# Optimization experiments

Hardware: AMD Instinct MI355X
Metric: run time of the kernel (lower is better)

## Reference

```python
import jax, jax.numpy as jnp
import numpy as np

D, H, O, E, K = 1024, 4096, 1024, 12, 4
N = 8192


def setup_inputs() -> dict:
    key = jax.random.key(0)
    ks = jax.random.split(key, 7)
    s = 0.02
    return {
        "x": jax.random.normal(ks[0], (N, D), dtype=jnp.float32),
        "gate_w": jax.random.normal(ks[1], (D, E), dtype=jnp.float32) * s,
        "gate_b": jnp.zeros((E,), dtype=jnp.float32),
        "w1": jax.random.normal(ks[2], (E, D, H), dtype=jnp.float32) * s,
        "b1": jnp.zeros((E, H), dtype=jnp.float32),
        "w2": jax.random.normal(ks[3], (E, H, O), dtype=jnp.float32) * s,
        "b2": jnp.zeros((E, O), dtype=jnp.float32),
    }


def reference(x, gate_w, gate_b, w1, b1, w2, b2):
    # Gating: full softmax over all experts, then mask to top-k and renormalize
    scores = x @ gate_w + gate_b                      # [N, E]
    _, topk_idx = jax.lax.top_k(scores, K)            # [N, K]
    mask = jnp.sum(jax.nn.one_hot(topk_idx, E, dtype=scores.dtype), axis=-2)  # [N, E]
    weights = jax.nn.softmax(scores, axis=-1) * mask
    weights = weights / (jnp.sum(weights, axis=-1, keepdims=True) + 1e-8)

    # Dense all-expert MLP (faithful to original: every expert on every token)
    h = jax.nn.relu(jnp.einsum("nd,edh->neh", x, w1) + b1)  # [N, E, H]
    outs = jnp.einsum("neh,eho->neo", h, w2) + b2           # [N, E, O]

    return jnp.einsum("ne,neo->no", weights, outs)          # [N, O]
```

## Files before the change

### kernel.cpp

```cpp
#include <hip/hip_runtime.h>
#include <stdint.h>

#define D_DIM 1024
#define H_DIM 4096
#define O_DIM 1024
#define E_NUM 12
#define TOPK 4
#define N_TOK 8192

#define PAIR_CAP 36096

typedef __bf16 bf16x8 __attribute__((ext_vector_type(8)));
typedef float f32x4 __attribute__((ext_vector_type(4)));
typedef unsigned short u16x8 __attribute__((ext_vector_type(8)));

typedef __attribute__((address_space(3))) unsigned int lds_uint;
typedef __attribute__((address_space(1))) const unsigned int glob_uint;

static __device__ __forceinline__ unsigned short f2b(float f) {
  union { float f; unsigned u; } v; v.f = f;
  unsigned r = v.u + 0x7FFFu + ((v.u >> 16) & 1u);
  return (unsigned short)(r >> 16);
}

static __device__ __forceinline__ void gload16(const void* g, void* l) {
  __builtin_amdgcn_global_load_lds((glob_uint*)g, (lds_uint*)l, 16, 0, 0);
}

__global__ __launch_bounds__(256) void cvt_x_kernel(const float* __restrict__ x,
                                                    unsigned short* __restrict__ xb) {
  int i = blockIdx.x * 256 + threadIdx.x;
  const float4* p = reinterpret_cast<const float4*>(x);
  float4 a = p[2 * i], b = p[2 * i + 1];
  uint4 st;
  st.x = (unsigned)f2b(a.x) | ((unsigned)f2b(a.y) << 16);
  st.y = (unsigned)f2b(a.z) | ((unsigned)f2b(a.w) << 16);
  st.z = (unsigned)f2b(b.x) | ((unsigned)f2b(b.y) << 16);
  st.w = (unsigned)f2b(b.z) | ((unsigned)f2b(b.w) << 16);
  reinterpret_cast<uint4*>(xb)[i] = st;
}

__global__ __launch_bounds__(256) void transpose_cvt_kernel(const float* __restrict__ in,
                                                            unsigned short* __restrict__ out,
                                                            int R, int C) {
  __shared__ float tile[64][33];
  int e = blockIdx.z;
  size_t base = (size_t)e * R * C;
  int c0 = blockIdx.x * 32, r0 = blockIdx.y * 64;
  int tx = threadIdx.x & 31, ty = threadIdx.x >> 5;
#pragma unroll
  for (int i = 0; i < 64; i += 8)
    tile[ty + i][tx] = in[base + (size_t)(r0 + ty + i) * C + (c0 + tx)];
  __syncthreads();
#pragma unroll
  for (int k = 0; k < 4; k++) {
    int c = ty + k * 8;
    unsigned lo = f2b(tile[2 * tx][c]);
    unsigned hi = f2b(tile[2 * tx + 1][c]);
    *reinterpret_cast<unsigned*>(&out[base + (size_t)(c0 + c) * R + r0 + 2 * tx]) =
        lo | (hi << 16);
  }
}

__global__ __launch_bounds__(256) void gwt_kernel(const float* __restrict__ gw,
                                                  float* __restrict__ gwT) {
  int e = blockIdx.x;
#pragma unroll
  for (int i = 0; i < 4; i++) {
    int d = i * 256 + threadIdx.x;
    gwT[e * D_DIM + d] = gw[(size_t)d * E_NUM + e];
  }
}

__global__ __launch_bounds__(256) void gating_kernel(const float* __restrict__ x,
                                                     const float* __restrict__ gwT,
                                                     const float* __restrict__ gb,
                                                     int* __restrict__ tk_e,
                                                     float* __restrict__ tk_w) {
  int wv = (blockIdx.x * 256 + threadIdx.x) >> 6;
  int lane = threadIdx.x & 63;
  int n0 = wv * 4;
  if (n0 >= N_TOK) return;

  const float4* x4 = reinterpret_cast<const float4*>(x);
  const float4* g4 = reinterpret_cast<const float4*>(gwT);

  float acc[4][E_NUM];
#pragma unroll
  for (int t = 0; t < 4; t++)
#pragma unroll
    for (int e = 0; e < E_NUM; e++) acc[t][e] = 0.f;

#pragma unroll
  for (int i = 0; i < 4; i++) {
    float4 xv[4];
#pragma unroll
    for (int t = 0; t < 4; t++) xv[t] = x4[(size_t)(n0 + t) * 256 + i * 64 + lane];
#pragma unroll
    for (int e = 0; e < E_NUM; e++) {
      float4 g = g4[e * 256 + i * 64 + lane];
#pragma unroll
      for (int t = 0; t < 4; t++)
        acc[t][e] += xv[t].x * g.x + xv[t].y * g.y + xv[t].z * g.z + xv[t].w * g.w;
    }
  }

#pragma unroll
  for (int t = 0; t < 4; t++)
#pragma unroll
    for (int e = 0; e < E_NUM; e++) {
      float v = acc[t][e];
#pragma unroll
      for (int s = 32; s > 0; s >>= 1) v += __shfl_xor(v, s, 64);
      acc[t][e] = v;
    }

#pragma unroll
  for (int t = 0; t < 4; t++) {
    if (lane == t) {
      int n = n0 + t;
      float sc[E_NUM], sm[E_NUM];
      float mx = -1e30f;
#pragma unroll
      for (int e = 0; e < E_NUM; e++) { sc[e] = acc[t][e] + gb[e]; mx = fmaxf(mx, sc[e]); }
      float Z = 0.f;
#pragma unroll
      for (int e = 0; e < E_NUM; e++) { sm[e] = expf(sc[e] - mx); Z += sm[e]; }
      bool used[E_NUM];
#pragma unroll
      for (int e = 0; e < E_NUM; e++) used[e] = false;
      int eid[TOPK]; float p[TOPK]; float wsum = 0.f;
      for (int k = 0; k < TOPK; k++) {
        float best = -1e30f; int bi = 0;
        for (int e = 0; e < E_NUM; e++)
          if (!used[e] && sc[e] > best) { best = sc[e]; bi = e; }
        used[bi] = true; eid[k] = bi; p[k] = sm[bi] / Z; wsum += p[k];
      }
      float inv = 1.f / (wsum + 1e-8f);
      for (int k = 0; k < TOPK; k++) {
        tk_e[n * TOPK + k] = eid[k];
        tk_w[n * TOPK + k] = p[k] * inv;
      }
    }
  }
}

__global__ __launch_bounds__(256) void hist_rank_kernel(const int* __restrict__ tk_e,
                                                        int* __restrict__ lr,
                                                        int* __restrict__ bc) {
  int blk = blockIdx.x, t = threadIdx.x;
  int n = blk * 256 + t;
  int4 te = reinterpret_cast<const int4*>(tk_e)[n];
  int lane = t & 63, w = t >> 6;
  __shared__ int wt[4][E_NUM];
  int r0 = 0, r1 = 0, r2 = 0, r3 = 0;
#pragma unroll
  for (int e = 0; e < E_NUM; e++) {
    int flag = (te.x == e) || (te.y == e) || (te.z == e) || (te.w == e);
    unsigned long long m = __ballot(flag);
    int rw = __popcll(m & ((1ull << lane) - 1ull));
    if (lane == 0) wt[w][e] = __popcll(m);
    if (te.x == e) r0 = rw;
    if (te.y == e) r1 = rw;
    if (te.z == e) r2 = rw;
    if (te.w == e) r3 = rw;
  }
  __syncthreads();
#pragma unroll
  for (int e = 0; e < E_NUM; e++) {
    int base = 0;
#pragma unroll
    for (int w2 = 0; w2 < 4; w2++)
      if (w2 < w) base += wt[w2][e];
    if (te.x == e) r0 += base;
    if (te.y == e) r1 += base;
    if (te.z == e) r2 += base;
    if (te.w == e) r3 += base;
  }
  int4 out; out.x = r0; out.y = r1; out.z = r2; out.w = r3;
  reinterpret_cast<int4*>(lr)[n] = out;
  if (t == 0) {
#pragma unroll
    for (int e = 0; e < E_NUM; e++)
      bc[blk * E_NUM + e] = wt[0][e] + wt[1][e] + wt[2][e] + wt[3][e];
  }
}

__global__ __launch_bounds__(64) void scan2_kernel(const int* __restrict__ bc,
                                                   int* __restrict__ poff,
                                                   int* __restrict__ bb) {
  int t = threadIdx.x;
  __shared__ int cnte[E_NUM];
  __shared__ int spoff[E_NUM + 1];
  if (t < E_NUM) {
    int s = 0;
#pragma unroll
    for (int b = 0; b < 32; b++) s += bc[b * E_NUM + t];
    cnte[t] = s;
  }
  __syncthreads();
  if (t == 0) {
    int off = 0; spoff[0] = 0;
    for (int e = 0; e < E_NUM; e++) {
      off += ((cnte[e] + 255) >> 8) << 8;
      spoff[e + 1] = off;
    }
  }
  __syncthreads();
  if (t < E_NUM + 1) poff[t] = spoff[t];
  if (t < E_NUM) {
    int run = spoff[t];
    for (int b = 0; b < 32; b++) {
      bb[b * E_NUM + t] = run;
      run += bc[b * E_NUM + t];
    }
  }
}

__global__ __launch_bounds__(256) void fill_pairs_kernel(int* __restrict__ pt) {
  int i = blockIdx.x * 256 + threadIdx.x;
  if (i < PAIR_CAP) pt[i] = 0;
}

__global__ __launch_bounds__(256) void scatter2_kernel(const int* __restrict__ tk_e,
                                                       int* __restrict__ lr_ip,
                                                       const int* __restrict__ bb,
                                                       int* __restrict__ pt) {
  int n = blockIdx.x * 256 + threadIdx.x;
  if (n >= N_TOK) return;
  int blk = n >> 8;
  int4 te = reinterpret_cast<const int4*>(tk_e)[n];
  int4 l4 = reinterpret_cast<const int4*>(lr_ip)[n];
  int p0 = bb[blk * E_NUM + te.x] + l4.x;
  int p1 = bb[blk * E_NUM + te.y] + l4.y;
  int p2 = bb[blk * E_NUM + te.z] + l4.z;
  int p3 = bb[blk * E_NUM + te.w] + l4.w;
  pt[p0] = n; pt[p1] = n; pt[p2] = n; pt[p3] = n;
  int4 ip; ip.x = p0; ip.y = p1; ip.z = p2; ip.w = p3;
  reinterpret_cast<int4*>(lr_ip)[n] = ip;
}


#define PHASE(MF0, EXTRA)                                                          \
  {                                                                                \
    bf16x8 af0k0 = *reinterpret_cast<const bf16x8*>(&Asl[((MF0) * 16 + fr) * 64 + aq0e]);     \
    bf16x8 af0k1 = *reinterpret_cast<const bf16x8*>(&Asl[((MF0) * 16 + fr) * 64 + aq1e]);     \
    bf16x8 af1k0 = *reinterpret_cast<const bf16x8*>(&Asl[((MF0) * 16 + 16 + fr) * 64 + aq0e]); \
    bf16x8 af1k1 = *reinterpret_cast<const bf16x8*>(&Asl[((MF0) * 16 + 16 + fr) * 64 + aq1e]); \
    EXTRA                                                                          \
    __builtin_amdgcn_s_barrier();                                                  \
    __builtin_amdgcn_s_setprio(1);                                                 \
    _Pragma("unroll")                                                              \
    for (int nf = 0; nf < 4; nf++) {                                               \
      acc[MF0][nf]     = __builtin_amdgcn_mfma_f32_16x16x32_bf16(af0k0, bfr[nf][0], acc[MF0][nf], 0, 0, 0);     \
      acc[MF0][nf]     = __builtin_amdgcn_mfma_f32_16x16x32_bf16(af0k1, bfr[nf][1], acc[MF0][nf], 0, 0, 0);     \
      acc[MF0 + 1][nf] = __builtin_amdgcn_mfma_f32_16x16x32_bf16(af1k0, bfr[nf][0], acc[MF0 + 1][nf], 0, 0, 0); \
      acc[MF0 + 1][nf] = __builtin_amdgcn_mfma_f32_16x16x32_bf16(af1k1, bfr[nf][1], acc[MF0 + 1][nf], 0, 0, 0); \
    }                                                                              \
    __builtin_amdgcn_s_setprio(0);                                                 \
  }

#define STAGE_A(sb, ko)                                       \
  gload16(aptr00 + (ko), &Ah[sb][0][tid * 8]);                \
  gload16(aptr01 + (ko), &Ah[sb][0][4096 + tid * 8]);         \
  gload16(aptr10 + (ko), &Ah[sb][1][tid * 8]);                \
  gload16(aptr11 + (ko), &Ah[sb][1][4096 + tid * 8]);
#define STAGE_B(sb, ko)                                       \
  gload16(bptr00 + (ko), &Bh[sb][0][tid * 8]);                \
  gload16(bptr01 + (ko), &Bh[sb][0][4096 + tid * 8]);         \
  gload16(bptr10 + (ko), &Bh[sb][1][tid * 8]);                \
  gload16(bptr11 + (ko), &Bh[sb][1][4096 + tid * 8]);

__global__ __launch_bounds__(512, 2) void gemm1_kernel(
    const unsigned short* __restrict__ xb,
    const unsigned short* __restrict__ w1t,
    const float* __restrict__ b1,
    const int* __restrict__ pair_token,
    const int* __restrict__ poff,
    unsigned short* __restrict__ hbuf,
    int tile0) {
  __shared__ unsigned short Ah[2][2][8192];
  __shared__ unsigned short Bh[2][2][8192];

  int cpx = gridDim.x >> 3;
  int f = (blockIdx.x & 7) * cpx + (blockIdx.x >> 3);
  int colb = f & 15;
  int tile = f >> 4;
  int t = tile0 + tile;
  int totTiles = poff[E_NUM] >> 8;
  if (t >= totTiles) return;
  int rowg0 = t << 8;
  int e = 0;
#pragma unroll
  for (int i = 1; i < E_NUM; i++) e += (rowg0 >= poff[i]);

  const int tid = threadIdx.x;
  const int lane = tid & 63, wave = tid >> 6;
  const int wm = wave >> 2, wn = wave & 3;
  const int fr = lane & 15, fgq = lane >> 4;
  const int frq = fr & 7;
  const int aq0e = (fgq ^ frq) << 3;
  const int aq1e = ((4 | fgq) ^ frq) << 3;
  const int brow = (wn & 1) << 6;

  const int srow = tid >> 3;
  const int cs = ((tid & 7) ^ (srow & 7)) << 3;

  const unsigned short* aptr00 = xb + (size_t)pair_token[rowg0 + srow] * D_DIM + cs;
  const unsigned short* aptr01 = xb + (size_t)pair_token[rowg0 + 64 + srow] * D_DIM + cs;
  const unsigned short* aptr10 = xb + (size_t)pair_token[rowg0 + 128 + srow] * D_DIM + cs;
  const unsigned short* aptr11 = xb + (size_t)pair_token[rowg0 + 192 + srow] * D_DIM + cs;
  int n0 = colb << 8;
  const unsigned short* wbb = w1t + (size_t)e * H_DIM * D_DIM;
  const unsigned short* bptr00 = wbb + (size_t)(n0 + srow) * D_DIM + cs;
  const unsigned short* bptr01 = wbb + (size_t)(n0 + 64 + srow) * D_DIM + cs;
  const unsigned short* bptr10 = wbb + (size_t)(n0 + 128 + srow) * D_DIM + cs;
  const unsigned short* bptr11 = wbb + (size_t)(n0 + 192 + srow) * D_DIM + cs;

  f32x4 acc[8][4];
#pragma unroll
  for (int i = 0; i < 8; i++)
#pragma unroll
    for (int j = 0; j < 4; j++) acc[i][j] = (f32x4){0.f, 0.f, 0.f, 0.f};

  STAGE_A(0, 0);
  STAGE_B(0, 0);
  for (int kt = 0; kt < D_DIM / 64; ++kt) {
    const int s = kt & 1;
    const int kon = (kt + 1) << 6;
    const unsigned short* Asl = Ah[s][wm];
    const unsigned short* Bsl = Bh[s][wn >> 1];
    __syncthreads();
    bf16x8 bfr[4][2];
#pragma unroll
    for (int nf = 0; nf < 4; nf++) {
      bfr[nf][0] = *reinterpret_cast<const bf16x8*>(&Bsl[(brow + nf * 16 + fr) * 64 + aq0e]);
      bfr[nf][1] = *reinterpret_cast<const bf16x8*>(&Bsl[(brow + nf * 16 + fr) * 64 + aq1e]);
    }
    if (kt + 1 < D_DIM / 64) {
      PHASE(0, STAGE_A(s ^ 1, kon));
      __builtin_amdgcn_s_barrier();
      PHASE(2, STAGE_B(s ^ 1, kon));
    } else {
      PHASE(0, );
      __builtin_amdgcn_s_barrier();
      PHASE(2, );
    }
    __builtin_amdgcn_s_barrier();
    PHASE(4, );
    __builtin_amdgcn_s_barrier();
    PHASE(6, );
  }

  int lrow0 = (tile << 8) + (wm << 7);
#pragma unroll
  for (int nf = 0; nf < 4; nf++) {
    int col = n0 + wn * 64 + nf * 16 + fr;
    float bias = b1[e * H_DIM + col];
#pragma unroll
    for (int mf = 0; mf < 8; mf++)
#pragma unroll
      for (int r = 0; r < 4; r++) {
        float v = fmaxf(acc[mf][nf][r] + bias, 0.f);
        hbuf[(size_t)(lrow0 + mf * 16 + fgq * 4 + r) * H_DIM + col] = f2b(v);
      }
  }
}

__global__ __launch_bounds__(512, 2) void gemm2_kernel(
    const unsigned short* __restrict__ hbuf,
    const unsigned short* __restrict__ w2t,
    const float* __restrict__ b2,
    const int* __restrict__ poff,
    unsigned short* __restrict__ youts,
    int tile0) {
  __shared__ unsigned short Ah[2][2][8192];
  __shared__ unsigned short Bh[2][2][8192];

  int cpx = gridDim.x >> 3;
  int f = (blockIdx.x & 7) * cpx + (blockIdx.x >> 3);
  int colb = f & 3;
  int z = (f >> 2) & 1;
  int tile = f >> 3;
  int t = tile0 + tile;
  int totTiles = poff[E_NUM] >> 8;
  if (t >= totTiles) return;
  int rowg0 = t << 8;
  int e = 0;
#pragma unroll
  for (int i = 1; i < E_NUM; i++) e += (rowg0 >= poff[i]);

  const int tid = threadIdx.x;
  const int lane = tid & 63, wave = tid >> 6;
  const int wm = wave >> 2, wn = wave & 3;
  const int fr = lane & 15, fgq = lane >> 4;
  const int frq = fr & 7;
  const int aq0e = (fgq ^ frq) << 3;
  const int aq1e = ((4 | fgq) ^ frq) << 3;
  const int brow = (wn & 1) << 6;

  const int srow = tid >> 3;
  const int cs = ((tid & 7) ^ (srow & 7)) << 3;
  const int kbase = z << 11;

  int lrowb = tile << 8;
  const unsigned short* aptr00 = hbuf + (size_t)(lrowb + srow) * H_DIM + kbase + cs;
  const unsigned short* aptr01 = hbuf + (size_t)(lrowb + 64 + srow) * H_DIM + kbase + cs;
  const unsigned short* aptr10 = hbuf + (size_t)(lrowb + 128 + srow) * H_DIM + kbase + cs;
  const unsigned short* aptr11 = hbuf + (size_t)(lrowb + 192 + srow) * H_DIM + kbase + cs;
  int n0 = colb << 8;
  const unsigned short* wbb = w2t + (size_t)e * O_DIM * H_DIM;
  const unsigned short* bptr00 = wbb + (size_t)(n0 + srow) * H_DIM + kbase + cs;
  const unsigned short* bptr01 = wbb + (size_t)(n0 + 64 + srow) * H_DIM + kbase + cs;
  const unsigned short* bptr10 = wbb + (size_t)(n0 + 128 + srow) * H_DIM + kbase + cs;
  const unsigned short* bptr11 = wbb + (size_t)(n0 + 192 + srow) * H_DIM + kbase + cs;

  f32x4 acc[8][4];
#pragma unroll
  for (int i = 0; i < 8; i++)
#pragma unroll
    for (int j = 0; j < 4; j++) acc[i][j] = (f32x4){0.f, 0.f, 0.f, 0.f};

  STAGE_A(0, 0);
  STAGE_B(0, 0);
  for (int kt = 0; kt < 32; ++kt) {
    const int s = kt & 1;
    const int kon = (kt + 1) << 6;
    const unsigned short* Asl = Ah[s][wm];
    const unsigned short* Bsl = Bh[s][wn >> 1];
    __syncthreads();
    bf16x8 bfr[4][2];
#pragma unroll
    for (int nf = 0; nf < 4; nf++) {
      bfr[nf][0] = *reinterpret_cast<const bf16x8*>(&Bsl[(brow + nf * 16 + fr) * 64 + aq0e]);
      bfr[nf][1] = *reinterpret_cast<const bf16x8*>(&Bsl[(brow + nf * 16 + fr) * 64 + aq1e]);
    }
    if (kt + 1 < 32) {
      PHASE(0, STAGE_A(s ^ 1, kon));
      __builtin_amdgcn_s_barrier();
      PHASE(2, STAGE_B(s ^ 1, kon));
    } else {
      PHASE(0, );
      __builtin_amdgcn_s_barrier();
      PHASE(2, );
    }
    __builtin_amdgcn_s_barrier();
    PHASE(4, );
    __builtin_amdgcn_s_barrier();
    PHASE(6, );
  }

  size_t ybase = (size_t)z * PAIR_CAP + rowg0 + (wm << 7);
#pragma unroll
  for (int nf = 0; nf < 4; nf++) {
    int col = n0 + wn * 64 + nf * 16 + fr;
    float bias = (z == 0) ? b2[e * O_DIM + col] : 0.f;
#pragma unroll
    for (int mf = 0; mf < 8; mf++)
#pragma unroll
      for (int r = 0; r < 4; r++) {
        float v = acc[mf][nf][r] + bias;
        youts[(ybase + mf * 16 + fgq * 4 + r) * O_DIM + col] = f2b(v);
      }
  }
}

static __device__ __forceinline__ void acc8(float* a, const unsigned short* y, float wk) {
  u16x8 v = *reinterpret_cast<const u16x8*>(y);
#pragma unroll
  for (int j = 0; j < 8; j++)
    a[j] += wk * __uint_as_float((unsigned)v[j] << 16);
}

__global__ __launch_bounds__(256) void reduce_kernel(const unsigned short* __restrict__ youts,
                                                     const int* __restrict__ ip,
                                                     const float* __restrict__ tk_w,
                                                     float* __restrict__ out) {
  int gid = blockIdx.x * 256 + threadIdx.x;
  int n = gid >> 7;
  int c0 = (gid & 127) << 3;
  int4 p = reinterpret_cast<const int4*>(ip)[n];
  float4 w = reinterpret_cast<const float4*>(tk_w)[n];
  const size_t zoff = (size_t)PAIR_CAP * O_DIM;
  float a[8];
#pragma unroll
  for (int j = 0; j < 8; j++) a[j] = 0.f;
  {
    const unsigned short* y = youts + (size_t)p.x * O_DIM + c0;
    acc8(a, y, w.x); acc8(a, y + zoff, w.x);
  }
  {
    const unsigned short* y = youts + (size_t)p.y * O_DIM + c0;
    acc8(a, y, w.y); acc8(a, y + zoff, w.y);
  }
  {
    const unsigned short* y = youts + (size_t)p.z * O_DIM + c0;
    acc8(a, y, w.z); acc8(a, y + zoff, w.z);
  }
  {
    const unsigned short* y = youts + (size_t)p.w * O_DIM + c0;
    acc8(a, y, w.w); acc8(a, y + zoff, w.w);
  }
  float* orow = out + (size_t)n * O_DIM + c0;
  float4 o0; o0.x = a[0]; o0.y = a[1]; o0.z = a[2]; o0.w = a[3];
  float4 o1; o1.x = a[4]; o1.y = a[5]; o1.z = a[6]; o1.w = a[7];
  reinterpret_cast<float4*>(orow)[0] = o0;
  reinterpret_cast<float4*>(orow)[1] = o1;
}

extern "C" void kernel_launch(void* const* d_in, const int* in_sizes, int n_in,
                              void* d_out, int out_size, void* d_ws, size_t ws_size,
                              hipStream_t stream) {
  const float* x  = (const float*)d_in[0];
  const float* gw = (const float*)d_in[1];
  const float* gb = (const float*)d_in[2];
  const float* w1 = (const float*)d_in[3];
  const float* b1 = (const float*)d_in[4];
  const float* w2 = (const float*)d_in[5];
  const float* b2 = (const float*)d_in[6];
  float* out = (float*)d_out;

  char* ws = (char*)d_ws;
  size_t off = 0;
  auto alloc = [&](size_t bytes) -> void* {
    void* p = ws + off;
    off = (off + bytes + 255) & ~(size_t)255;
    return p;
  };
  unsigned short* xb   = (unsigned short*)alloc((size_t)N_TOK * D_DIM * 2);
  unsigned short* w1t  = (unsigned short*)alloc((size_t)E_NUM * H_DIM * D_DIM * 2);
  unsigned short* w2t  = (unsigned short*)alloc((size_t)E_NUM * O_DIM * H_DIM * 2);
  float* gwT  = (float*)alloc((size_t)E_NUM * D_DIM * 4);
  int*   tk_e = (int*)alloc((size_t)N_TOK * TOPK * 4);
  float* tk_w = (float*)alloc((size_t)N_TOK * TOPK * 4);
  int*   lr   = (int*)alloc((size_t)N_TOK * TOPK * 4);
  int*   pt   = (int*)alloc((size_t)PAIR_CAP * 4);
  int*   bc   = (int*)alloc(32 * E_NUM * 4);
  int*   bb   = (int*)alloc(32 * E_NUM * 4);
  int*   poff = (int*)alloc(64);

  const size_t YO2 = (size_t)2 * PAIR_CAP * O_DIM * 2;
  auto need = [&](int tpcN) {
    return off + (size_t)tpcN * 256 * H_DIM * 2 + YO2 + 2048;
  };
  int TPC, NCH;
  if (ws_size >= need(141))      { TPC = 141; NCH = 1; }
  else if (ws_size >= need(71))  { TPC = 71;  NCH = 2; }
  else                           { TPC = 47;  NCH = 3; }
  unsigned short* hbuf  = (unsigned short*)alloc((size_t)TPC * 256 * H_DIM * 2);
  unsigned short* youts = (unsigned short*)alloc(YO2);
  if (off > ws_size) return;

  cvt_x_kernel<<<N_TOK * D_DIM / 8 / 256, 256, 0, stream>>>(x, xb);
  transpose_cvt_kernel<<<dim3(H_DIM / 32, D_DIM / 64, E_NUM), 256, 0, stream>>>(w1, w1t, D_DIM, H_DIM);
  transpose_cvt_kernel<<<dim3(O_DIM / 32, H_DIM / 64, E_NUM), 256, 0, stream>>>(w2, w2t, H_DIM, O_DIM);
  gwt_kernel<<<E_NUM, 256, 0, stream>>>(gw, gwT);
  gating_kernel<<<N_TOK / 16, 256, 0, stream>>>(x, gwT, gb, tk_e, tk_w);
  hist_rank_kernel<<<N_TOK / 256, 256, 0, stream>>>(tk_e, lr, bc);
  scan2_kernel<<<1, 64, 0, stream>>>(bc, poff, bb);
  fill_pairs_kernel<<<(PAIR_CAP + 255) / 256, 256, 0, stream>>>(pt);
  scatter2_kernel<<<N_TOK / 256, 256, 0, stream>>>(tk_e, lr, bb, pt);

  for (int c = 0; c < NCH; c++) {
    int tile0 = c * TPC;
    gemm1_kernel<<<dim3(16 * TPC), 512, 0, stream>>>(xb, w1t, b1, pt, poff, hbuf, tile0);
    gemm2_kernel<<<dim3(8 * TPC), 512, 0, stream>>>(hbuf, w2t, b2, poff, youts, tile0);
  }
  reduce_kernel<<<N_TOK * (O_DIM / 8) / 256, 256, 0, stream>>>(youts, lr, tk_w, out);
}
```

Baseline: 996.8 us.

## Issue next-tile global loads upfront with vmcnt waits; chunk GEMMs into smaller tile groups

```diff
diff --git a/kernel.cpp b/kernel.cpp
--- a/kernel.cpp
+++ b/kernel.cpp
@@ -241,13 +241,12 @@
 }
 
 
-#define PHASE(MF0, EXTRA)                                                          \
+#define PHASE(MF0)                                                                 \
   {                                                                                \
     bf16x8 af0k0 = *reinterpret_cast<const bf16x8*>(&Asl[((MF0) * 16 + fr) * 64 + aq0e]);     \
     bf16x8 af0k1 = *reinterpret_cast<const bf16x8*>(&Asl[((MF0) * 16 + fr) * 64 + aq1e]);     \
     bf16x8 af1k0 = *reinterpret_cast<const bf16x8*>(&Asl[((MF0) * 16 + 16 + fr) * 64 + aq0e]); \
     bf16x8 af1k1 = *reinterpret_cast<const bf16x8*>(&Asl[((MF0) * 16 + 16 + fr) * 64 + aq1e]); \
-    EXTRA                                                                          \
     __builtin_amdgcn_s_barrier();                                                  \
     __builtin_amdgcn_s_setprio(1);                                                 \
     _Pragma("unroll")                                                              \
@@ -271,6 +270,37 @@
   gload16(bptr10 + (ko), &Bh[sb][1][tid * 8]);                \
   gload16(bptr11 + (ko), &Bh[sb][1][4096 + tid * 8]);
 
+#define KLOOP(NT)                                                                  \
+  STAGE_A(0, 0);                                                                   \
+  STAGE_B(0, 0);                                                                   \
+  for (int kt = 0; kt < (NT); ++kt) {                                              \
+    const int s = kt & 1;                                                          \
+    const unsigned short* Asl = Ah[s][wm];                                         \
+    const unsigned short* Bsl = Bh[s][wn >> 1];                                    \
+    if (kt + 1 < (NT)) {                                                           \
+      const int kon = (kt + 1) << 6;                                               \
+      STAGE_A(s ^ 1, kon);                                                         \
+      STAGE_B(s ^ 1, kon);                                                         \
+      asm volatile("s_waitcnt vmcnt(8)" ::: "memory");                             \
+    } else {                                                                       \
+      asm volatile("s_waitcnt vmcnt(0)" ::: "memory");                             \
+    }                                                                              \
+    __builtin_amdgcn_s_barrier();                                                  \
+    bf16x8 bfr[4][2];                                                              \
+    _Pragma("unroll")                                                              \
+    for (int nf = 0; nf < 4; nf++) {                                               \
+      bfr[nf][0] = *reinterpret_cast<const bf16x8*>(&Bsl[(brow + nf * 16 + fr) * 64 + aq0e]); \
+      bfr[nf][1] = *reinterpret_cast<const bf16x8*>(&Bsl[(brow + nf * 16 + fr) * 64 + aq1e]); \
+    }                                                                              \
+    PHASE(0);                                                                      \
+    __builtin_amdgcn_s_barrier();                                                  \
+    PHASE(2);                                                                      \
+    __builtin_amdgcn_s_barrier();                                                  \
+    PHASE(4);                                                                      \
+    __builtin_amdgcn_s_barrier();                                                  \
+    PHASE(6);                                                                      \
+  }
+
 __global__ __launch_bounds__(512, 2) void gemm1_kernel(
     const unsigned short* __restrict__ xb,
     const unsigned short* __restrict__ w1t,
@@ -323,34 +353,7 @@
 #pragma unroll
     for (int j = 0; j < 4; j++) acc[i][j] = (f32x4){0.f, 0.f, 0.f, 0.f};
 
-  STAGE_A(0, 0);
-  STAGE_B(0, 0);
-  for (int kt = 0; kt < D_DIM / 64; ++kt) {
-    const int s = kt & 1;
-    const int kon = (kt + 1) << 6;
-    const unsigned short* Asl = Ah[s][wm];
-    const unsigned short* Bsl = Bh[s][wn >> 1];
-    __syncthreads();
-    bf16x8 bfr[4][2];
-#pragma unroll
-    for (int nf = 0; nf < 4; nf++) {
-      bfr[nf][0] = *reinterpret_cast<const bf16x8*>(&Bsl[(brow + nf * 16 + fr) * 64 + aq0e]);
-      bfr[nf][1] = *reinterpret_cast<const bf16x8*>(&Bsl[(brow + nf * 16 + fr) * 64 + aq1e]);
-    }
-    if (kt + 1 < D_DIM / 64) {
-      PHASE(0, STAGE_A(s ^ 1, kon));
-      __builtin_amdgcn_s_barrier();
-      PHASE(2, STAGE_B(s ^ 1, kon));
-    } else {
-      PHASE(0, );
-      __builtin_amdgcn_s_barrier();
-      PHASE(2, );
-    }
-    __builtin_amdgcn_s_barrier();
-    PHASE(4, );
-    __builtin_amdgcn_s_barrier();
-    PHASE(6, );
-  }
+  KLOOP(D_DIM / 64);
 
   int lrow0 = (tile << 8) + (wm << 7);
 #pragma unroll
@@ -421,34 +424,7 @@
 #pragma unroll
     for (int j = 0; j < 4; j++) acc[i][j] = (f32x4){0.f, 0.f, 0.f, 0.f};
 
-  STAGE_A(0, 0);
-  STAGE_B(0, 0);
-  for (int kt = 0; kt < 32; ++kt) {
-    const int s = kt & 1;
-    const int kon = (kt + 1) << 6;
-    const unsigned short* Asl = Ah[s][wm];
-    const unsigned short* Bsl = Bh[s][wn >> 1];
-    __syncthreads();
-    bf16x8 bfr[4][2];
-#pragma unroll
-    for (int nf = 0; nf < 4; nf++) {
-      bfr[nf][0] = *reinterpret_cast<const bf16x8*>(&Bsl[(brow + nf * 16 + fr) * 64 + aq0e]);
-      bfr[nf][1] = *reinterpret_cast<const bf16x8*>(&Bsl[(brow + nf * 16 + fr) * 64 + aq1e]);
-    }
-    if (kt + 1 < 32) {
-      PHASE(0, STAGE_A(s ^ 1, kon));
-      __builtin_amdgcn_s_barrier();
-      PHASE(2, STAGE_B(s ^ 1, kon));
-    } else {
-      PHASE(0, );
-      __builtin_amdgcn_s_barrier();
-      PHASE(2, );
-    }
-    __builtin_amdgcn_s_barrier();
-    PHASE(4, );
-    __builtin_amdgcn_s_barrier();
-    PHASE(6, );
-  }
+  KLOOP(32);
 
   size_t ybase = (size_t)z * PAIR_CAP + rowg0 + (wm << 7);
 #pragma unroll
@@ -544,9 +520,9 @@
     return off + (size_t)tpcN * 256 * H_DIM * 2 + YO2 + 2048;
   };
   int TPC, NCH;
-  if (ws_size >= need(141))      { TPC = 141; NCH = 1; }
-  else if (ws_size >= need(71))  { TPC = 71;  NCH = 2; }
-  else                           { TPC = 47;  NCH = 3; }
+  if (ws_size >= need(71))       { TPC = 71; NCH = 2; }
+  else if (ws_size >= need(47))  { TPC = 47; NCH = 3; }
+  else                           { TPC = 24; NCH = 6; }
   unsigned short* hbuf  = (unsigned short*)alloc((size_t)TPC * 256 * H_DIM * 2);
   unsigned short* youts = (unsigned short*)alloc(YO2);
   if (off > ws_size) return;
```

After: 1.194 ms. 19.8% more time.
